# Kernel optimization log

Measured on AMD Instinct MI355X. Metric: run time of the kernel, lower is better.

## Reference

```python
import jax, jax.numpy as jnp
import numpy as np

N_NODES = 16384
N_EDGES = 131072
MUL = 64                # multiplicity of 0e and 1o node irreps
N_RADIAL = 8
HIDDEN = 64
NUM_IRREPS = 6 * MUL    # 192x0e + 192x1o after concat/regroup
AVG_NUM_NEIGHBORS = 8.0
INV_SQRT3 = 1.0 / np.sqrt(3.0)  # wigner-3j(1,1,0) component normalization


def setup_inputs() -> dict:
    key = jax.random.key(0)
    ks = jax.random.split(key, 8)
    return {
        "node_feats": jax.random.normal(ks[0], (N_NODES, MUL + 3 * MUL), jnp.float32),
        "edge_features": jax.random.normal(ks[1], (N_EDGES, 4), jnp.float32),
        "radial_embedding": jax.random.uniform(ks[2], (N_EDGES, N_RADIAL), jnp.float32),
        "w1": jax.random.normal(ks[3], (N_RADIAL, HIDDEN), jnp.float32),
        "w2": jax.random.normal(ks[4], (HIDDEN, HIDDEN), jnp.float32),
        "w3": jax.random.normal(ks[5], (HIDDEN, NUM_IRREPS), jnp.float32),
        "senders": jax.random.randint(ks[6], (N_EDGES,), 0, N_NODES),
        "receivers": jax.random.randint(ks[7], (N_EDGES,), 0, N_NODES),
    }


def reference(node_feats, edge_features, radial_embedding, w1, w2, w3, senders, receivers):
    N = node_feats.shape[0]
    E = senders.shape[0]
    # split node irreps: 64x0e (scalars) + 64x1o (vectors)
    s = node_feats[:, :MUL]                       # [N, 64]
    v = node_feats[:, MUL:].reshape(N, MUL, 3)    # [N, 64, 3]
    # gather by sender
    s_e = s[senders]                              # [E, 64]
    v_e = v[senders]                              # [E, 64, 3]
    # edge attrs: 1x0e + 1x1o (spherical harmonics l<=1)
    es = edge_features[:, :1]                     # [E, 1]
    ev = edge_features[:, 1:4]                    # [E, 3]
    # CG tensor product filtered to {0e, 1o} (component normalization)
    tp_s1 = s_e * es                                              # 0e x 0e -> 0e
    tp_s2 = jnp.einsum("emc,ec->em", v_e, ev) * INV_SQRT3        # 1o x 1o -> 0e
    tp_v1 = s_e[:, :, None] * ev[:, None, :]                      # 0e x 1o -> 1o
    tp_v2 = v_e * es[:, :, None]                                  # 1o x 0e -> 1o
    # concat(filtered node feats, tp output) regrouped -> 192x0e + 192x1o
    scal = jnp.concatenate([s_e, tp_s1, tp_s2], axis=1)          # [E, 192]
    vec = jnp.concatenate([v_e, tp_v1, tp_v2], axis=1)           # [E, 192, 3]
    # radial MLP (no bias, e3nn 1/sqrt(fan_in) scaling, no output activation)
    h = jax.nn.silu(radial_embedding @ w1 / np.sqrt(N_RADIAL))
    h = jax.nn.silu(h @ w2 / np.sqrt(HIDDEN))
    w = h @ w3 / np.sqrt(HIDDEN)                                  # [E, 384]
    n_scal = scal.shape[1]
    scal = scal * w[:, :n_scal]
    vec = vec * w[:, n_scal:, None]
    # scatter-add into receivers
    out_s = jnp.zeros((N, n_scal), scal.dtype).at[receivers].add(scal)
    out_v = jnp.zeros((N, n_scal, 3), vec.dtype).at[receivers].add(vec)
    out = jnp.concatenate([out_s, out_v.reshape(N, n_scal * 3)], axis=1)
    return out / np.sqrt(AVG_NUM_NEIGHBORS)
```

## Files before the change

### kernel.cpp

```cpp
#include <hip/hip_runtime.h>

#define N_NODES 16384
#define N_EDGES 131072
#define NUM_IRREPS 384
#define TE 64

#define INV_SQRT3   0.5773502691896258f
#define INV_SQRT8   0.35355339059327373f
#define SC3         (0.125f * 0.35355339059327373f)

typedef __attribute__((ext_vector_type(8))) __bf16 bf16x8;
typedef __attribute__((ext_vector_type(8))) unsigned short ushort8;
typedef __attribute__((ext_vector_type(4))) float f32x4;

union FragU { ushort8 u; bf16x8 b; };

__device__ __forceinline__ float silu_f(float x) {
    return x / (1.0f + __expf(-x));
}
__device__ __forceinline__ unsigned short bf16_rn(float f) {
    union { float f; unsigned int u; } c; c.f = f;
    unsigned int u = c.u + 0x7FFFu + ((c.u >> 16) & 1u);
    return (unsigned short)(u >> 16);
}
__device__ __forceinline__ float bf16_to_f(unsigned short h) {
    union { unsigned int u; float f; } c; c.u = ((unsigned int)h) << 16;
    return c.f;
}

__global__ __launch_bounds__(256) void pack_kernel(
    const float* __restrict__ w2, const float* __restrict__ w3,
    unsigned short* __restrict__ w2p, unsigned short* __restrict__ w3p)
{
    int t = blockIdx.x * 256 + threadIdx.x;
    float v;
    unsigned short *hi_dst, *lo_dst;
    if (t < 4096) {
        int K = t >> 11, T = (t >> 9) & 3, lane = (t >> 3) & 63, j = t & 7;
        int k = K * 32 + (lane >> 4) * 8 + j;
        int n = T * 16 + (lane & 15);
        v = w2[k * 64 + n] * 0.125f;
        hi_dst = w2p + t; lo_dst = w2p + 4096 + t;
    } else if (t < 28672) {
        int u = t - 4096;
        int K = u / 12288; int rem = u - K * 12288;
        int T = rem >> 9, lane = (rem >> 3) & 63, j = rem & 7;
        int k = K * 32 + (lane >> 4) * 8 + j;
        int n = T * 16 + (lane & 15);
        v = w3[k * 384 + n] * SC3;
        hi_dst = w3p + u; lo_dst = w3p + 24576 + u;
    } else {
        return;
    }
    unsigned short h = bf16_rn(v);
    unsigned short l = bf16_rn(v - bf16_to_f(h));
    *hi_dst = h; *lo_dst = l;
}

__global__ __launch_bounds__(256) void hist_kernel(
    const int* __restrict__ receivers, int* __restrict__ counts)
{
    int e = blockIdx.x * 256 + threadIdx.x;
    if (e < N_EDGES) atomicAdd(&counts[receivers[e]], 1);
}

__global__ __launch_bounds__(256) void scan_kernel(
    const int* __restrict__ counts, int* __restrict__ offsets,
    int* __restrict__ cursor)
{
    __shared__ int sums[256];
    __shared__ int excl[256];
    const int t = threadIdx.x;
    const int base = t * 64;
    int s = 0;
    for (int i = 0; i < 64; ++i) s += counts[base + i];
    sums[t] = s;
    __syncthreads();
    if (t == 0) {
        int r = 0;
        for (int i = 0; i < 256; ++i) { excl[i] = r; r += sums[i]; }
    }
    __syncthreads();
    int run = excl[t];
    for (int i = 0; i < 64; ++i) {
        offsets[base + i] = run;
        cursor[base + i]  = run;
        run += counts[base + i];
    }
    if (t == 255) offsets[N_NODES] = run;
}

__global__ __launch_bounds__(256) void fill_kernel(
    const int* __restrict__ receivers, int* __restrict__ cursor,
    int* __restrict__ sorted)
{
    int e = blockIdx.x * 256 + threadIdx.x;
    if (e < N_EDGES) {
        int pos = atomicAdd(&cursor[receivers[e]], 1);
        sorted[pos] = e;
    }
}

__global__ __launch_bounds__(256) void mlp_kernel(
    const float* __restrict__ radial,
    const float* __restrict__ w1,
    const unsigned short* __restrict__ w2p,
    const unsigned short* __restrict__ w3p,
    const int* __restrict__ sorted,
    unsigned short* __restrict__ wout,
    int p_begin)
{
    __shared__ float w1s[512];
    __shared__ float rs[64 * 9];
    __shared__ float h1s[64 * 68];
    __shared__ float h2s[64 * 68];

    const int t   = threadIdx.x;
    const int le0 = blockIdx.x * TE;
    const int p0  = p_begin + le0;

    for (int i = t; i < 512; i += 256) w1s[i] = w1[i];
    if (t < 128) {
        int j = t >> 1, half = t & 1;
        int eid = sorted[p0 + j];
        float4 rv = *(const float4*)&radial[(size_t)eid * 8 + half * 4];
        float* d = &rs[j * 9 + half * 4];
        d[0] = rv.x; d[1] = rv.y; d[2] = rv.z; d[3] = rv.w;
    }
    __syncthreads();

    {
        const int e  = t >> 2;
        const int j0 = (t & 3) * 16;
        float acc[16];
#pragma unroll
        for (int j = 0; j < 16; ++j) acc[j] = 0.0f;
#pragma unroll
        for (int k = 0; k < 8; ++k) {
            float rv = rs[e * 9 + k];
#pragma unroll
            for (int j = 0; j < 16; ++j)
                acc[j] += rv * w1s[k * 64 + j0 + j];
        }
#pragma unroll
        for (int j = 0; j < 16; ++j)
            h1s[e * 68 + j0 + j] = silu_f(acc[j] * INV_SQRT8);
    }
    __syncthreads();

    const int lane = t & 63;
    const int wv   = t >> 6;
    const int m0   = wv * 16;
    const int quad = lane >> 4;
    const int l15  = lane & 15;

    FragU ah[2], al[2];

#pragma unroll
    for (int K = 0; K < 2; ++K) {
        const float4* p = (const float4*)&h1s[(m0 + l15) * 68 + K * 32 + quad * 8];
        float4 x0 = p[0], x1 = p[1];
        float xs[8] = {x0.x, x0.y, x0.z, x0.w, x1.x, x1.y, x1.z, x1.w};
#pragma unroll
        for (int j = 0; j < 8; ++j) {
            unsigned short h = bf16_rn(xs[j]);
            ah[K].u[j] = h;
            al[K].u[j] = bf16_rn(xs[j] - bf16_to_f(h));
        }
    }

#pragma unroll
    for (int T = 0; T < 4; ++T) {
        FragU bh0, bh1, bl0, bl1;
        bh0.u = *(const ushort8*)(w2p +        T * 512 + lane * 8);
        bh1.u = *(const ushort8*)(w2p + 2048 + T * 512 + lane * 8);
        bl0.u = *(const ushort8*)(w2p + 4096 + T * 512 + lane * 8);
        bl1.u = *(const ushort8*)(w2p + 6144 + T * 512 + lane * 8);
        f32x4 acc = {0.f, 0.f, 0.f, 0.f};
        acc = __builtin_amdgcn_mfma_f32_16x16x32_bf16(ah[0].b, bh0.b, acc, 0, 0, 0);
        acc = __builtin_amdgcn_mfma_f32_16x16x32_bf16(ah[1].b, bh1.b, acc, 0, 0, 0);
        acc = __builtin_amdgcn_mfma_f32_16x16x32_bf16(ah[0].b, bl0.b, acc, 0, 0, 0);
        acc = __builtin_amdgcn_mfma_f32_16x16x32_bf16(ah[1].b, bl1.b, acc, 0, 0, 0);
        acc = __builtin_amdgcn_mfma_f32_16x16x32_bf16(al[0].b, bh0.b, acc, 0, 0, 0);
        acc = __builtin_amdgcn_mfma_f32_16x16x32_bf16(al[1].b, bh1.b, acc, 0, 0, 0);
#pragma unroll
        for (int r = 0; r < 4; ++r)
            h2s[(m0 + quad * 4 + r) * 68 + T * 16 + l15] = silu_f(acc[r]);
    }
    __syncthreads();

#pragma unroll
    for (int K = 0; K < 2; ++K) {
        const float4* p = (const float4*)&h2s[(m0 + l15) * 68 + K * 32 + quad * 8];
        float4 x0 = p[0], x1 = p[1];
        float xs[8] = {x0.x, x0.y, x0.z, x0.w, x1.x, x1.y, x1.z, x1.w};
#pragma unroll
        for (int j = 0; j < 8; ++j) {
            unsigned short h = bf16_rn(xs[j]);
            ah[K].u[j] = h;
            al[K].u[j] = bf16_rn(xs[j] - bf16_to_f(h));
        }
    }

    for (int T = 0; T < 24; ++T) {
        FragU bh0, bh1, bl0, bl1;
        bh0.u = *(const ushort8*)(w3p +         T * 512 + lane * 8);
        bh1.u = *(const ushort8*)(w3p + 12288 + T * 512 + lane * 8);
        bl0.u = *(const ushort8*)(w3p + 24576 + T * 512 + lane * 8);
        bl1.u = *(const ushort8*)(w3p + 36864 + T * 512 + lane * 8);
        f32x4 acc = {0.f, 0.f, 0.f, 0.f};
        acc = __builtin_amdgcn_mfma_f32_16x16x32_bf16(ah[0].b, bh0.b, acc, 0, 0, 0);
        acc = __builtin_amdgcn_mfma_f32_16x16x32_bf16(ah[1].b, bh1.b, acc, 0, 0, 0);
        acc = __builtin_amdgcn_mfma_f32_16x16x32_bf16(ah[0].b, bl0.b, acc, 0, 0, 0);
        acc = __builtin_amdgcn_mfma_f32_16x16x32_bf16(ah[1].b, bl1.b, acc, 0, 0, 0);
        acc = __builtin_amdgcn_mfma_f32_16x16x32_bf16(al[0].b, bh0.b, acc, 0, 0, 0);
        acc = __builtin_amdgcn_mfma_f32_16x16x32_bf16(al[1].b, bh1.b, acc, 0, 0, 0);
#pragma unroll
        for (int r = 0; r < 4; ++r)
            wout[(size_t)(le0 + m0 + quad * 4 + r) * 384 + T * 16 + l15] = bf16_rn(acc[r]);
    }
}

__global__ __launch_bounds__(256) void accum_kernel(
    const float* __restrict__ node_feats,
    const float* __restrict__ edge_features,
    const unsigned short* __restrict__ wbuf,
    const int* __restrict__ senders,
    const int* __restrict__ sorted,
    const int* __restrict__ offsets,
    float* __restrict__ out,
    int p0, int cnt)
{
    const int n    = blockIdx.x;
    const int wid  = threadIdx.x >> 6;
    const int lane = threadIdx.x & 63;
    const int beg  = offsets[n];
    const int end  = offsets[n + 1];

    float as0 = 0.f, as1 = 0.f, as2 = 0.f;
    float av[3][3] = {};

    for (int i = beg + wid; i < end; i += 4) {
        if (i < p0 || i >= p0 + cnt) continue;

        const int e     = sorted[i];
        const int sidx  = senders[e];
        const float es  = edge_features[e * 4 + 0];
        const float ev0 = edge_features[e * 4 + 1];
        const float ev1 = edge_features[e * 4 + 2];
        const float ev2 = edge_features[e * 4 + 3];

        const float* nf = node_feats + (size_t)sidx * 256;
        const float s  = nf[lane];
        const float v0 = nf[64 + lane * 3 + 0];
        const float v1 = nf[64 + lane * 3 + 1];
        const float v2 = nf[64 + lane * 3 + 2];

        const unsigned short* wp = wbuf + (size_t)(i - p0) * 384;
        const float ws0 = bf16_to_f(wp[lane]);
        const float ws1 = bf16_to_f(wp[64 + lane]);
        const float ws2 = bf16_to_f(wp[128 + lane]);
        const float wv0 = bf16_to_f(wp[192 + lane]);
        const float wv1 = bf16_to_f(wp[256 + lane]);
        const float wv2 = bf16_to_f(wp[320 + lane]);

        const float dot = (v0 * ev0 + v1 * ev1 + v2 * ev2) * INV_SQRT3;

        as0 += s * ws0;
        as1 += s * es * ws1;
        as2 += dot * ws2;

        av[0][0] += v0 * wv0; av[0][1] += v1 * wv0; av[0][2] += v2 * wv0;
        const float sw = s * wv1;
        av[1][0] += ev0 * sw; av[1][1] += ev1 * sw; av[1][2] += ev2 * sw;
        const float esw = es * wv2;
        av[2][0] += v0 * esw; av[2][1] += v1 * esw; av[2][2] += v2 * esw;
    }

    __shared__ float red[4 * 768];
    float* my = red + wid * 768;
    my[lane]        = as0;
    my[64 + lane]   = as1;
    my[128 + lane]  = as2;
#pragma unroll
    for (int c = 0; c < 3; ++c) {
        const int b = 192 + (c * 64 + lane) * 3;
        my[b + 0] = av[c][0];
        my[b + 1] = av[c][1];
        my[b + 2] = av[c][2];
    }
    __syncthreads();

    float* orow = out + (size_t)n * 768;
    for (int j = threadIdx.x; j < 768; j += 256) {
        float v = red[j] + red[768 + j] + red[1536 + j] + red[2304 + j];
        if (p0 == 0) orow[j] = v;
        else         orow[j] += v;
    }
}

extern "C" void kernel_launch(void* const* d_in, const int* in_sizes, int n_in,
                              void* d_out, int out_size, void* d_ws, size_t ws_size,
                              hipStream_t stream) {
    const float* node_feats    = (const float*)d_in[0];
    const float* edge_features = (const float*)d_in[1];
    const float* radial        = (const float*)d_in[2];
    const float* w1            = (const float*)d_in[3];
    const float* w2            = (const float*)d_in[4];
    const float* w3            = (const float*)d_in[5];
    const int*   senders       = (const int*)d_in[6];
    const int*   receivers     = (const int*)d_in[7];
    float* out = (float*)d_out;

    int* counts  = (int*)d_ws;
    int* offsets = counts + N_NODES;
    int* cursor  = offsets + N_NODES + 1;
    int* sorted  = cursor + N_NODES;
    size_t int_bytes = (size_t)((char*)(sorted + N_EDGES) - (char*)d_ws);
    size_t pk_off = (int_bytes + 255) & ~(size_t)255;
    unsigned short* w2p = (unsigned short*)((char*)d_ws + pk_off);
    unsigned short* w3p = w2p + 8192;
    size_t wbuf_off = (pk_off + (8192 + 49152) * sizeof(unsigned short) + 255) & ~(size_t)255;
    unsigned short* wbuf = (unsigned short*)((char*)d_ws + wbuf_off);

    hipMemsetAsync(counts, 0, (size_t)N_NODES * sizeof(int), stream);
    hist_kernel<<<(N_EDGES + 255) / 256, 256, 0, stream>>>(receivers, counts);
    pack_kernel<<<112, 256, 0, stream>>>(w2, w3, w2p, w3p);
    scan_kernel<<<1, 256, 0, stream>>>(counts, offsets, cursor);
    fill_kernel<<<(N_EDGES + 255) / 256, 256, 0, stream>>>(receivers, cursor, sorted);

    size_t avail = (ws_size > wbuf_off) ? (ws_size - wbuf_off) : 0;
    size_t max_chunk = avail / (NUM_IRREPS * sizeof(unsigned short));
    max_chunk &= ~(size_t)(TE - 1);
    int chunk = (max_chunk >= (size_t)N_EDGES) ? N_EDGES
              : (max_chunk < (size_t)TE ? TE : (int)max_chunk);

    for (int p0 = 0; p0 < N_EDGES; p0 += chunk) {
        int cnt = N_EDGES - p0;
        if (cnt > chunk) cnt = chunk;
        int nb1 = (cnt + TE - 1) / TE;
        mlp_kernel<<<nb1, 256, 0, stream>>>(radial, w1, w2p, w3p, sorted, wbuf, p0);
        accum_kernel<<<N_NODES, 256, 0, stream>>>(node_feats, edge_features, wbuf,
                                                  senders, sorted, offsets, out, p0, cnt);
    }
}
```

Before: 202.6 us.

## Double MLP edge tile, one wave per node in accum, fold memset into pack

The MLP kernel now processes 128 edges per block, with each wave computing two 16-row MFMA tiles so each loaded B fragment is used twice. The accumulation kernel assigns one wavefront per receiver node, processes its edges serially and writes directly to global memory, dropping the shared-memory reduction and block barrier. The counts memset moves into the pack kernel, and the scan uses wave shuffles instead of a serial single-thread pass. Serial per-node loops lose edge-level parallelism for high-degree nodes, and fewer MLP blocks reduce occupancy.

```diff
diff --git a/kernel.cpp b/kernel.cpp
--- a/kernel.cpp
+++ b/kernel.cpp
@@ -3,7 +3,7 @@
 #define N_NODES 16384
 #define N_EDGES 131072
 #define NUM_IRREPS 384
-#define TE 64
+#define TE 128
 
 #define INV_SQRT3   0.5773502691896258f
 #define INV_SQRT8   0.35355339059327373f
@@ -30,9 +30,11 @@
 
 __global__ __launch_bounds__(256) void pack_kernel(
     const float* __restrict__ w2, const float* __restrict__ w3,
-    unsigned short* __restrict__ w2p, unsigned short* __restrict__ w3p)
+    unsigned short* __restrict__ w2p, unsigned short* __restrict__ w3p,
+    int* __restrict__ counts)
 {
     int t = blockIdx.x * 256 + threadIdx.x;
+    if (t < N_NODES) counts[t] = 0;
     float v;
     unsigned short *hi_dst, *lo_dst;
     if (t < 4096) {
@@ -68,20 +70,23 @@
     const int* __restrict__ counts, int* __restrict__ offsets,
     int* __restrict__ cursor)
 {
-    __shared__ int sums[256];
-    __shared__ int excl[256];
-    const int t = threadIdx.x;
+    __shared__ int wsum[4];
+    const int t    = threadIdx.x;
+    const int lane = t & 63;
+    const int wv   = t >> 6;
     const int base = t * 64;
     int s = 0;
     for (int i = 0; i < 64; ++i) s += counts[base + i];
-    sums[t] = s;
-    __syncthreads();
-    if (t == 0) {
-        int r = 0;
-        for (int i = 0; i < 256; ++i) { excl[i] = r; r += sums[i]; }
-    }
-    __syncthreads();
-    int run = excl[t];
+    const int own = s;
+    for (int off = 1; off < 64; off <<= 1) {
+        int v = __shfl_up(s, off, 64);
+        if (lane >= off) s += v;
+    }
+    if (lane == 63) wsum[wv] = s;
+    __syncthreads();
+    int pre = 0;
+    for (int j = 0; j < wv; ++j) pre += wsum[j];
+    int run = pre + s - own;
     for (int i = 0; i < 64; ++i) {
         offsets[base + i] = run;
         cursor[base + i]  = run;
@@ -99,6 +104,37 @@
         int pos = atomicAdd(&cursor[receivers[e]], 1);
         sorted[pos] = e;
     }
+}
+
+__device__ __forceinline__ void build_afrags(
+    const float* __restrict__ hs, int row, int quad, FragU (&ah)[2], FragU (&al)[2])
+{
+#pragma unroll
+    for (int K = 0; K < 2; ++K) {
+        const float4* p = (const float4*)&hs[row * 68 + K * 32 + quad * 8];
+        float4 x0 = p[0], x1 = p[1];
+        float xs[8] = {x0.x, x0.y, x0.z, x0.w, x1.x, x1.y, x1.z, x1.w};
+#pragma unroll
+        for (int j = 0; j < 8; ++j) {
+            unsigned short h = bf16_rn(xs[j]);
+            ah[K].u[j] = h;
+            al[K].u[j] = bf16_rn(xs[j] - bf16_to_f(h));
+        }
+    }
+}
+
+__device__ __forceinline__ f32x4 mfma6(
+    const FragU (&ah)[2], const FragU (&al)[2],
+    const FragU& bh0, const FragU& bh1, const FragU& bl0, const FragU& bl1,
+    f32x4 acc)
+{
+    acc = __builtin_amdgcn_mfma_f32_16x16x32_bf16(ah[0].b, bh0.b, acc, 0, 0, 0);
+    acc = __builtin_amdgcn_mfma_f32_16x16x32_bf16(ah[1].b, bh1.b, acc, 0, 0, 0);
+    acc = __builtin_amdgcn_mfma_f32_16x16x32_bf16(ah[0].b, bl0.b, acc, 0, 0, 0);
+    acc = __builtin_amdgcn_mfma_f32_16x16x32_bf16(ah[1].b, bl1.b, acc, 0, 0, 0);
+    acc = __builtin_amdgcn_mfma_f32_16x16x32_bf16(al[0].b, bh0.b, acc, 0, 0, 0);
+    acc = __builtin_amdgcn_mfma_f32_16x16x32_bf16(al[1].b, bh1.b, acc, 0, 0, 0);
+    return acc;
 }
 
 __global__ __launch_bounds__(256) void mlp_kernel(
@@ -111,26 +147,28 @@
     int p_begin)
 {
     __shared__ float w1s[512];
-    __shared__ float rs[64 * 9];
-    __shared__ float h1s[64 * 68];
-    __shared__ float h2s[64 * 68];
+    __shared__ float rs[TE * 9];
+    __shared__ float h1s[TE * 68];
+    __shared__ float h2s[TE * 68];
+    __shared__ int eids[TE];
 
     const int t   = threadIdx.x;
     const int le0 = blockIdx.x * TE;
     const int p0  = p_begin + le0;
 
     for (int i = t; i < 512; i += 256) w1s[i] = w1[i];
-    if (t < 128) {
+    if (t < TE) eids[t] = sorted[p0 + t];
+    __syncthreads();
+    {
         int j = t >> 1, half = t & 1;
-        int eid = sorted[p0 + j];
-        float4 rv = *(const float4*)&radial[(size_t)eid * 8 + half * 4];
+        float4 rv = *(const float4*)&radial[(size_t)eids[j] * 8 + half * 4];
         float* d = &rs[j * 9 + half * 4];
         d[0] = rv.x; d[1] = rv.y; d[2] = rv.z; d[3] = rv.w;
     }
     __syncthreads();
 
-    {
-        const int e  = t >> 2;
+    for (int h = 0; h < 2; ++h) {
+        const int e  = h * 64 + (t >> 2);
         const int j0 = (t & 3) * 16;
         float acc[16];
 #pragma unroll
@@ -150,24 +188,15 @@
 
     const int lane = t & 63;
     const int wv   = t >> 6;
-    const int m0   = wv * 16;
+    const int mA   = wv * 16;
+    const int mB   = mA + 64;
     const int quad = lane >> 4;
     const int l15  = lane & 15;
 
-    FragU ah[2], al[2];
-
-#pragma unroll
-    for (int K = 0; K < 2; ++K) {
-        const float4* p = (const float4*)&h1s[(m0 + l15) * 68 + K * 32 + quad * 8];
-        float4 x0 = p[0], x1 = p[1];
-        float xs[8] = {x0.x, x0.y, x0.z, x0.w, x1.x, x1.y, x1.z, x1.w};
-#pragma unroll
-        for (int j = 0; j < 8; ++j) {
-            unsigned short h = bf16_rn(xs[j]);
-            ah[K].u[j] = h;
-            al[K].u[j] = bf16_rn(xs[j] - bf16_to_f(h));
-        }
-    }
+    FragU ahA[2], alA[2], ahB[2], alB[2];
+
+    build_afrags(h1s, mA + l15, quad, ahA, alA);
+    build_afrags(h1s, mB + l15, quad, ahB, alB);
 
 #pragma unroll
     for (int T = 0; T < 4; ++T) {
@@ -176,31 +205,20 @@
         bh1.u = *(const ushort8*)(w2p + 2048 + T * 512 + lane * 8);
         bl0.u = *(const ushort8*)(w2p + 4096 + T * 512 + lane * 8);
         bl1.u = *(const ushort8*)(w2p + 6144 + T * 512 + lane * 8);
-        f32x4 acc = {0.f, 0.f, 0.f, 0.f};
-        acc = __builtin_amdgcn_mfma_f32_16x16x32_bf16(ah[0].b, bh0.b, acc, 0, 0, 0);
-        acc = __builtin_amdgcn_mfma_f32_16x16x32_bf16(ah[1].b, bh1.b, acc, 0, 0, 0);
-        acc = __builtin_amdgcn_mfma_f32_16x16x32_bf16(ah[0].b, bl0.b, acc, 0, 0, 0);
-        acc = __builtin_amdgcn_mfma_f32_16x16x32_bf16(ah[1].b, bl1.b, acc, 0, 0, 0);
-        acc = __builtin_amdgcn_mfma_f32_16x16x32_bf16(al[0].b, bh0.b, acc, 0, 0, 0);
-        acc = __builtin_amdgcn_mfma_f32_16x16x32_bf16(al[1].b, bh1.b, acc, 0, 0, 0);
-#pragma unroll
-        for (int r = 0; r < 4; ++r)
-            h2s[(m0 + quad * 4 + r) * 68 + T * 16 + l15] = silu_f(acc[r]);
-    }
-    __syncthreads();
-
-#pragma unroll
-    for (int K = 0; K < 2; ++K) {
-        const float4* p = (const float4*)&h2s[(m0 + l15) * 68 + K * 32 + quad * 8];
-        float4 x0 = p[0], x1 = p[1];
-        float xs[8] = {x0.x, x0.y, x0.z, x0.w, x1.x, x1.y, x1.z, x1.w};
-#pragma unroll
-        for (int j = 0; j < 8; ++j) {
-            unsigned short h = bf16_rn(xs[j]);
-            ah[K].u[j] = h;
-            al[K].u[j] = bf16_rn(xs[j] - bf16_to_f(h));
+        f32x4 aA = {0.f, 0.f, 0.f, 0.f};
+        f32x4 aB = {0.f, 0.f, 0.f, 0.f};
+        aA = mfma6(ahA, alA, bh0, bh1, bl0, bl1, aA);
+        aB = mfma6(ahB, alB, bh0, bh1, bl0, bl1, aB);
+#pragma unroll
+        for (int r = 0; r < 4; ++r) {
+            h2s[(mA + quad * 4 + r) * 68 + T * 16 + l15] = silu_f(aA[r]);
+            h2s[(mB + quad * 4 + r) * 68 + T * 16 + l15] = silu_f(aB[r]);
         }
     }
+    __syncthreads();
+
+    build_afrags(h2s, mA + l15, quad, ahA, alA);
+    build_afrags(h2s, mB + l15, quad, ahB, alB);
 
     for (int T = 0; T < 24; ++T) {
         FragU bh0, bh1, bl0, bl1;
@@ -208,16 +226,15 @@
         bh1.u = *(const ushort8*)(w3p + 12288 + T * 512 + lane * 8);
         bl0.u = *(const ushort8*)(w3p + 24576 + T * 512 + lane * 8);
         bl1.u = *(const ushort8*)(w3p + 36864 + T * 512 + lane * 8);
-        f32x4 acc = {0.f, 0.f, 0.f, 0.f};
-        acc = __builtin_amdgcn_mfma_f32_16x16x32_bf16(ah[0].b, bh0.b, acc, 0, 0, 0);
-        acc = __builtin_amdgcn_mfma_f32_16x16x32_bf16(ah[1].b, bh1.b, acc, 0, 0, 0);
-        acc = __builtin_amdgcn_mfma_f32_16x16x32_bf16(ah[0].b, bl0.b, acc, 0, 0, 0);
-        acc = __builtin_amdgcn_mfma_f32_16x16x32_bf16(ah[1].b, bl1.b, acc, 0, 0, 0);
-        acc = __builtin_amdgcn_mfma_f32_16x16x32_bf16(al[0].b, bh0.b, acc, 0, 0, 0);
-        acc = __builtin_amdgcn_mfma_f32_16x16x32_bf16(al[1].b, bh1.b, acc, 0, 0, 0);
-#pragma unroll
-        for (int r = 0; r < 4; ++r)
-            wout[(size_t)(le0 + m0 + quad * 4 + r) * 384 + T * 16 + l15] = bf16_rn(acc[r]);
+        f32x4 aA = {0.f, 0.f, 0.f, 0.f};
+        f32x4 aB = {0.f, 0.f, 0.f, 0.f};
+        aA = mfma6(ahA, alA, bh0, bh1, bl0, bl1, aA);
+        aB = mfma6(ahB, alB, bh0, bh1, bl0, bl1, aB);
+#pragma unroll
+        for (int r = 0; r < 4; ++r) {
+            wout[(size_t)(le0 + mA + quad * 4 + r) * 384 + T * 16 + l15] = bf16_rn(aA[r]);
+            wout[(size_t)(le0 + mB + quad * 4 + r) * 384 + T * 16 + l15] = bf16_rn(aB[r]);
+        }
     }
 }
 
@@ -231,16 +248,16 @@
     float* __restrict__ out,
     int p0, int cnt)
 {
-    const int n    = blockIdx.x;
-    const int wid  = threadIdx.x >> 6;
     const int lane = threadIdx.x & 63;
+    const int n    = blockIdx.x * 4 + (threadIdx.x >> 6);
     const int beg  = offsets[n];
     const int end  = offsets[n + 1];
 
-    float as0 = 0.f, as1 = 0.f, as2 = 0.f;
-    float av[3][3] = {};
-
-    for (int i = beg + wid; i < end; i += 4) {
+    float a[12];
+#pragma unroll
+    for (int j = 0; j < 12; ++j) a[j] = 0.f;
+
+    for (int i = beg; i < end; ++i) {
         if (i < p0 || i >= p0 + cnt) continue;
 
         const int e     = sorted[i];
@@ -266,36 +283,34 @@
 
         const float dot = (v0 * ev0 + v1 * ev1 + v2 * ev2) * INV_SQRT3;
 
-        as0 += s * ws0;
-        as1 += s * es * ws1;
-        as2 += dot * ws2;
-
-        av[0][0] += v0 * wv0; av[0][1] += v1 * wv0; av[0][2] += v2 * wv0;
+        a[0] += s * ws0;
+        a[1] += s * es * ws1;
+        a[2] += dot * ws2;
+        a[3] += v0 * wv0; a[4] += v1 * wv0; a[5] += v2 * wv0;
         const float sw = s * wv1;
-        av[1][0] += ev0 * sw; av[1][1] += ev1 * sw; av[1][2] += ev2 * sw;
+        a[6] += ev0 * sw; a[7] += ev1 * sw; a[8] += ev2 * sw;
         const float esw = es * wv2;
-        av[2][0] += v0 * esw; av[2][1] += v1 * esw; av[2][2] += v2 * esw;
-    }
-
-    __shared__ float red[4 * 768];
-    float* my = red + wid * 768;
-    my[lane]        = as0;
-    my[64 + lane]   = as1;
-    my[128 + lane]  = as2;
-#pragma unroll
-    for (int c = 0; c < 3; ++c) {
-        const int b = 192 + (c * 64 + lane) * 3;
-        my[b + 0] = av[c][0];
-        my[b + 1] = av[c][1];
-        my[b + 2] = av[c][2];
-    }
-    __syncthreads();
+        a[9] += v0 * esw; a[10] += v1 * esw; a[11] += v2 * esw;
+    }
 
     float* orow = out + (size_t)n * 768;
-    for (int j = threadIdx.x; j < 768; j += 256) {
-        float v = red[j] + red[768 + j] + red[1536 + j] + red[2304 + j];
-        if (p0 == 0) orow[j] = v;
-        else         orow[j] += v;
+    const int b0 = 192 + lane * 3;
+    const int b1 = 192 + (64 + lane) * 3;
+    const int b2 = 192 + (128 + lane) * 3;
+    if (p0 == 0) {
+        orow[lane]       = a[0];
+        orow[64 + lane]  = a[1];
+        orow[128 + lane] = a[2];
+        orow[b0 + 0] = a[3]; orow[b0 + 1] = a[4];  orow[b0 + 2] = a[5];
+        orow[b1 + 0] = a[6]; orow[b1 + 1] = a[7];  orow[b1 + 2] = a[8];
+        orow[b2 + 0] = a[9]; orow[b2 + 1] = a[10]; orow[b2 + 2] = a[11];
+    } else {
+        orow[lane]       += a[0];
+        orow[64 + lane]  += a[1];
+        orow[128 + lane] += a[2];
+        orow[b0 + 0] += a[3]; orow[b0 + 1] += a[4];  orow[b0 + 2] += a[5];
+        orow[b1 + 0] += a[6]; orow[b1 + 1] += a[7];  orow[b1 + 2] += a[8];
+        orow[b2 + 0] += a[9]; orow[b2 + 1] += a[10]; orow[b2 + 2] += a[11];
     }
 }
 
@@ -323,9 +338,8 @@
     size_t wbuf_off = (pk_off + (8192 + 49152) * sizeof(unsigned short) + 255) & ~(size_t)255;
     unsigned short* wbuf = (unsigned short*)((char*)d_ws + wbuf_off);
 
-    hipMemsetAsync(counts, 0, (size_t)N_NODES * sizeof(int), stream);
+    pack_kernel<<<112, 256, 0, stream>>>(w2, w3, w2p, w3p, counts);
     hist_kernel<<<(N_EDGES + 255) / 256, 256, 0, stream>>>(receivers, counts);
-    pack_kernel<<<112, 256, 0, stream>>>(w2, w3, w2p, w3p);
     scan_kernel<<<1, 256, 0, stream>>>(counts, offsets, cursor);
     fill_kernel<<<(N_EDGES + 255) / 256, 256, 0, stream>>>(receivers, cursor, sorted);
 
@@ -340,7 +354,7 @@
         if (cnt > chunk) cnt = chunk;
         int nb1 = (cnt + TE - 1) / TE;
         mlp_kernel<<<nb1, 256, 0, stream>>>(radial, w1, w2p, w3p, sorted, wbuf, p0);
-        accum_kernel<<<N_NODES, 256, 0, stream>>>(node_feats, edge_features, wbuf,
-                                                  senders, sorted, offsets, out, p0, cnt);
-    }
-}
+        accum_kernel<<<N_NODES / 4, 256, 0, stream>>>(node_feats, edge_features, wbuf,
+                                                      senders, sorted, offsets, out, p0, cnt);
+    }
+}
```

New measurement: 202.8 us. About the same (+0.1%).
